# Performance work log

Measured on AMD Instinct MI355X. Metric: run time of the kernel, lower is better.

Reference implementation:

```python
import jax, jax.numpy as jnp
import numpy as np

EMBED = 1024
HEADS = 16
HEAD_DIM = EMBED // HEADS
N, SEQ = 8, 1024


def setup_inputs() -> dict:
    key = jax.random.key(0)
    ks = jax.random.split(key, 9)
    values = jax.random.normal(ks[0], (N, SEQ, EMBED), dtype=jnp.float32)
    keys_ = jax.random.normal(ks[1], (N, SEQ, EMBED), dtype=jnp.float32)
    query = jax.random.normal(ks[2], (N, SEQ, EMBED), dtype=jnp.float32)
    mask = jax.random.randint(ks[3], (N, 1, SEQ, SEQ), 0, 2, dtype=jnp.int32)
    s = 1.0 / np.sqrt(HEAD_DIM)
    Wv = jax.random.normal(ks[4], (HEAD_DIM, HEAD_DIM), dtype=jnp.float32) * s
    Wk = jax.random.normal(ks[5], (HEAD_DIM, HEAD_DIM), dtype=jnp.float32) * s
    Wq = jax.random.normal(ks[6], (HEAD_DIM, HEAD_DIM), dtype=jnp.float32) * s
    Wo = jax.random.normal(ks[7], (EMBED, EMBED), dtype=jnp.float32) * (1.0 / np.sqrt(EMBED))
    bo = jax.random.normal(ks[8], (EMBED,), dtype=jnp.float32) * 0.01
    return {"values": values, "keys": keys_, "query": query, "mask": mask,
            "Wv": Wv, "Wk": Wk, "Wq": Wq, "Wo": Wo, "bo": bo}


def reference(values, keys, query, mask, Wv, Wk, Wq, Wo, bo):
    n, q_len = query.shape[0], query.shape[1]
    v_len, k_len = values.shape[1], keys.shape[1]
    # reshape to (N, len, H, Dh); per-head linear projections share a (Dh,Dh) weight.
    v = values.reshape(n, v_len, HEADS, HEAD_DIM)
    k = keys.reshape(n, k_len, HEADS, HEAD_DIM)
    q = query.reshape(n, q_len, HEADS, HEAD_DIM)
    # torch Linear: x @ W.T
    v = jnp.einsum('nlhd,ed->nlhe', v, Wv)
    k = jnp.einsum('nlhd,ed->nlhe', k, Wk)
    q = jnp.einsum('nlhd,ed->nlhe', q, Wq)
    # scores (N,H,Q,K); mask BEFORE scaling, exactly as the torch module does
    att = jnp.einsum('nqhd,nkhd->nhqk', q, k)
    att = jnp.where(mask == 0, jnp.float32(-1e20), att)
    att = jax.nn.softmax(att / jnp.sqrt(jnp.float32(EMBED)), axis=3)
    out = jnp.einsum('nhql,nlhd->nqhd', att, v).reshape(n, q_len, EMBED)
    return out @ Wo.T + bo
```

## Files before the change

kernel.cpp:

```cpp
#include <hip/hip_runtime.h>
#include <hip/hip_bf16.h>

using bf16x8 = __attribute__((ext_vector_type(8))) __bf16;
using f32x4  = __attribute__((ext_vector_type(4))) float;

#define NB 8
#define SEQ 1024
#define HEADS 16
#define HD 64
#define EMB 1024

#if __has_builtin(__builtin_amdgcn_exp2f)
  #define EXPD(x) __builtin_amdgcn_exp2f(x)
  #define QSCALE  0.04508422f
  #define MASKV  -4.5084e18f
#else
  #define EXPD(x) __expf(x)
  #define QSCALE  0.03125f
  #define MASKV  -3.125e18f
#endif

__device__ __forceinline__ int cvtpk_bf16(float lo, float hi) {
    int r;
    asm("v_cvt_pk_bf16_f32 %0, %1, %2" : "=v"(r) : "v"(lo), "v"(hi));
    return r;
}

__device__ __forceinline__ void gld16(const __bf16* g, __bf16* l) {
    __builtin_amdgcn_global_load_lds((const __attribute__((address_space(1))) void*)g,
                                     (__attribute__((address_space(3))) void*)l, 16, 0, 0);
}

__global__ __launch_bounds__(256) void mask_pack(const int* __restrict__ mask,
                                                 unsigned long long* __restrict__ mp)
{
    const int row = blockIdx.x, n = blockIdx.y, t = threadIdx.x;
    const int w = t >> 6, lane = t & 63;
    const int* m = mask + ((size_t)n * SEQ + row) * SEQ;
    #pragma unroll
    for (int i = 0; i < 4; ++i) {
        unsigned long long b = __ballot(m[i * 256 + w * 64 + lane] != 0);
        if (lane == 0) mp[((size_t)n * SEQ + row) * 16 + i * 4 + w] = b;
    }
}

__global__ __launch_bounds__(256, 4) void proj_mfma(
    const float* __restrict__ q_in, const float* __restrict__ k_in, const float* __restrict__ v_in,
    const float* __restrict__ Wq, const float* __restrict__ Wk, const float* __restrict__ Wv,
    __bf16* __restrict__ qp, __bf16* __restrict__ kp, __bf16* __restrict__ vpt)
{
    const int z = blockIdx.z;
    const float* X  = (z == 0) ? q_in : (z == 1) ? k_in : v_in;
    const float* Wf = (z == 0) ? Wq   : (z == 1) ? Wk   : Wv;

    __shared__ __align__(16) __bf16 Wb[64 * 72];
    __shared__ __align__(16) __bf16 Xb[64 * 72];
    const int t = threadIdx.x;
    const int nh = blockIdx.y, n = nh >> 4, h = nh & 15;
    const int l0 = blockIdx.x * 64;
    for (int i = t; i < 4096; i += 256)
        Wb[(i >> 6) * 72 + (i & 63)] = (__bf16)Wf[i];
    {
        const int row = t >> 2, seg = (t & 3) * 16;
        const float* src = X + ((size_t)(n * SEQ + l0 + row)) * EMB + h * 64 + seg;
        union { __bf16 b[16]; uint4 u[2]; } tmp;
        #pragma unroll
        for (int jj = 0; jj < 4; ++jj) {
            float4 f = ((const float4*)src)[jj];
            tmp.b[jj*4+0] = (__bf16)f.x; tmp.b[jj*4+1] = (__bf16)f.y;
            tmp.b[jj*4+2] = (__bf16)f.z; tmp.b[jj*4+3] = (__bf16)f.w;
        }
        *(uint4*)&Xb[row * 72 + seg]     = tmp.u[0];
        *(uint4*)&Xb[row * 72 + seg + 8] = tmp.u[1];
    }
    __syncthreads();
    const int w = t >> 6, lane = t & 63, quad = lane >> 4, lr = lane & 15;
    bf16x8 af[2];
    #pragma unroll
    for (int ks = 0; ks < 2; ++ks)
        af[ks] = *(const bf16x8*)&Xb[(w * 16 + lr) * 72 + ks * 32 + quad * 8];
    const f32x4 zero4 = {0.f, 0.f, 0.f, 0.f};
    f32x4 acc[4];
    #pragma unroll
    for (int et = 0; et < 4; ++et) {
        acc[et] = zero4;
        #pragma unroll
        for (int ks = 0; ks < 2; ++ks) {
            bf16x8 bfrag = *(const bf16x8*)&Wb[(et * 16 + lr) * 72 + ks * 32 + quad * 8];
            acc[et] = __builtin_amdgcn_mfma_f32_16x16x32_bf16(af[ks], bfrag, acc[et], 0, 0, 0);
        }
    }
    if (z == 0) {
        #pragma unroll
        for (int et = 0; et < 4; ++et) acc[et] *= QSCALE;
    }
    __syncthreads();
    if (z < 2) {
        #pragma unroll
        for (int et = 0; et < 4; ++et)
            #pragma unroll
            for (int rr = 0; rr < 4; ++rr)
                Xb[(w * 16 + quad * 4 + rr) * 72 + et * 16 + lr] = (__bf16)acc[et][rr];
        __syncthreads();
        const int row = t >> 2, seg = (t & 3) * 16;
        uint4 a = *(uint4*)&Xb[row * 72 + seg];
        uint4 b = *(uint4*)&Xb[row * 72 + seg + 8];
        __bf16* outp = (z == 0) ? qp : kp;
        __bf16* dst = outp + (size_t)nh * 65536 + (size_t)(l0 + row) * 64 + seg;
        *(uint4*)&dst[0] = a;
        *(uint4*)&dst[8] = b;
    } else {
        #pragma unroll
        for (int et = 0; et < 4; ++et)
            #pragma unroll
            for (int rr = 0; rr < 4; ++rr)
                Xb[(et * 16 + lr) * 72 + w * 16 + quad * 4 + rr] = (__bf16)acc[et][rr];
        __syncthreads();
        const int e = t >> 2, seg = (t & 3) * 16;
        uint4 a = *(uint4*)&Xb[e * 72 + seg];
        uint4 b = *(uint4*)&Xb[e * 72 + seg + 8];
        __bf16* dst = vpt + (size_t)nh * 65536 + (size_t)e * SEQ + l0 + seg;
        *(uint4*)&dst[0] = a;
        *(uint4*)&dst[8] = b;
    }
}

__global__ __launch_bounds__(256, 4) void attn_mfma(
    const __bf16* __restrict__ qp, const __bf16* __restrict__ kp, const __bf16* __restrict__ vpt,
    const unsigned long long* __restrict__ mp, __bf16* __restrict__ attn_out)
{
    __shared__ __align__(16) __bf16 KV[2][2][64 * 64];
    const int t = threadIdx.x, w = t >> 6, lane = t & 63, quad = lane >> 4, lr = lane & 15;
    const int bid = blockIdx.x;
    const int nh = bid & 127, qg = bid >> 7;
    const int n = nh >> 4, h = nh & 15;
    const int q0 = qg * 128;
    const __bf16* Q  = qp  + (size_t)nh * 65536;
    const __bf16* K  = kp  + (size_t)nh * 65536;
    const __bf16* VT = vpt + (size_t)nh * 65536;

    int qrow[2];
    bf16x8 qf[2][2];
    const unsigned long long* mrow[2];
    #pragma unroll
    for (int g = 0; g < 2; ++g) {
        qrow[g] = q0 + g * 64 + w * 16 + lr;
        qf[g][0] = *(const bf16x8*)&Q[(size_t)qrow[g] * 64 + quad * 8];
        qf[g][1] = *(const bf16x8*)&Q[(size_t)qrow[g] * 64 + 32 + quad * 8];
        mrow[g] = mp + ((size_t)n * SEQ + qrow[g]) * 16;
    }

    const int srow = t >> 3, sc8 = t & 7;
    const int sswz = (sc8 ^ (srow & 7)) * 8;
    const int kofs = srow * 64 + sswz;
    const int vofs = srow * SEQ + sswz;

    auto issue = [&](int kc) {
        const int b = kc & 1;
        __bf16* kb = (__bf16*)&KV[b][0][0];
        __bf16* vb = (__bf16*)&KV[b][1][0];
        const __bf16* ksrc = K  + (size_t)kc * 4096 + kofs;
        const __bf16* vsrc = VT + (size_t)kc * 64   + vofs;
        gld16(ksrc,            kb + t * 8);
        gld16(ksrc + 32 * 64,  kb + t * 8 + 2048);
        gld16(vsrc,            vb + t * 8);
        gld16(vsrc + 32 * SEQ, vb + t * 8 + 2048);
    };

    const int s0 = ((quad ^ (lr & 7))) * 8;
    const int s1 = s0 ^ 32;

    const f32x4 zero4 = {0.f, 0.f, 0.f, 0.f};
    f32x4 O[2][4];
    #pragma unroll
    for (int g = 0; g < 2; ++g)
        #pragma unroll
        for (int mt = 0; mt < 4; ++mt) O[g][mt] = zero4;
    float l_part[2] = {0.f, 0.f};

    issue(0);
    for (int kc = 0; kc < 16; ++kc) {
        __syncthreads();
        if (kc + 1 < 16) issue(kc + 1);
        const unsigned long long mw0 = mrow[0][kc], mw1 = mrow[1][kc];
        const __bf16* Kb = (const __bf16*)&KV[kc & 1][0][0];
        const __bf16* Vb = (const __bf16*)&KV[kc & 1][1][0];

        f32x4 S[2][4];
        #pragma unroll
        for (int g = 0; g < 2; ++g)
            #pragma unroll
            for (int kt = 0; kt < 4; ++kt) S[g][kt] = zero4;
        __builtin_amdgcn_s_setprio(1);
        #pragma unroll
        for (int kt = 0; kt < 4; ++kt) {
            bf16x8 kf0 = *(const bf16x8*)&Kb[(kt * 16 + lr) * 64 + s0];
            bf16x8 kf1 = *(const bf16x8*)&Kb[(kt * 16 + lr) * 64 + s1];
            S[0][kt] = __builtin_amdgcn_mfma_f32_16x16x32_bf16(kf0, qf[0][0], S[0][kt], 0, 0, 0);
            S[1][kt] = __builtin_amdgcn_mfma_f32_16x16x32_bf16(kf0, qf[1][0], S[1][kt], 0, 0, 0);
            S[0][kt] = __builtin_amdgcn_mfma_f32_16x16x32_bf16(kf1, qf[0][1], S[0][kt], 0, 0, 0);
            S[1][kt] = __builtin_amdgcn_mfma_f32_16x16x32_bf16(kf1, qf[1][1], S[1][kt], 0, 0, 0);
        }
        __builtin_amdgcn_s_setprio(0);

        bf16x8 pf[2][2];
        #pragma unroll
        for (int g = 0; g < 2; ++g) {
            const unsigned long long mword = g ? mw1 : mw0;
            const unsigned int mlo = (unsigned int)(mword >> (quad * 4));
            const unsigned int mhi = (unsigned int)(mword >> (32 + quad * 4));
            float ev[16];
            float lsum = 0.f;
            #pragma unroll
            for (int kt = 0; kt < 4; ++kt)
                #pragma unroll
                for (int r = 0; r < 4; ++r) {
                    unsigned int bits = (kt < 2) ? mlo : mhi;
                    int sh = (kt & 1) * 16 + r;
                    float sv = ((bits >> sh) & 1u) ? S[g][kt][r] : MASKV;
                    float e = EXPD(sv);
                    lsum += e;
                    ev[kt * 4 + r] = e;
                }
            l_part[g] += lsum;
            #pragma unroll
            for (int ks = 0; ks < 2; ++ks) {
                const int ka = (2 * ks) * 4, kb2 = (2 * ks + 1) * 4;
                int d0 = cvtpk_bf16(ev[ka + 0], ev[ka + 1]);
                int d1 = cvtpk_bf16(ev[ka + 2], ev[ka + 3]);
                int d2 = cvtpk_bf16(ev[kb2 + 0], ev[kb2 + 1]);
                int d3 = cvtpk_bf16(ev[kb2 + 2], ev[kb2 + 3]);
                asm("v_permlane32_swap_b32 %0, %1" : "+v"(d0), "+v"(d2));
                asm("v_permlane16_swap_b32 %0, %1" : "+v"(d0), "+v"(d2));
                asm("v_permlane32_swap_b32 %0, %1" : "+v"(d1), "+v"(d3));
                asm("v_permlane16_swap_b32 %0, %1" : "+v"(d1), "+v"(d3));
                union { int di[4]; bf16x8 v; } pb;
                pb.di[0] = d0; pb.di[1] = d1; pb.di[2] = d2; pb.di[3] = d3;
                pf[g][ks] = pb.v;
            }
        }

        __builtin_amdgcn_s_setprio(1);
        #pragma unroll
        for (int ks = 0; ks < 2; ++ks) {
            const int sv = ks ? s1 : s0;
            #pragma unroll
            for (int mt = 0; mt < 4; ++mt) {
                bf16x8 vf = *(const bf16x8*)&Vb[(mt * 16 + lr) * 64 + sv];
                O[0][mt] = __builtin_amdgcn_mfma_f32_16x16x32_bf16(vf, pf[0][ks], O[0][mt], 0, 0, 0);
                O[1][mt] = __builtin_amdgcn_mfma_f32_16x16x32_bf16(vf, pf[1][ks], O[1][mt], 0, 0, 0);
            }
        }
        __builtin_amdgcn_s_setprio(0);
    }
    #pragma unroll
    for (int g = 0; g < 2; ++g) {
        float l = l_part[g];
        l += __shfl_xor(l, 16, 64);
        l += __shfl_xor(l, 32, 64);
        const float linv = 1.0f / l;
        #pragma unroll
        for (int mt = 0; mt < 4; ++mt) {
            union { __bf16 b[4]; uint2 u; } pk;
            #pragma unroll
            for (int r = 0; r < 4; ++r) pk.b[r] = (__bf16)(O[g][mt][r] * linv);
            *(uint2*)&attn_out[((size_t)n * SEQ + qrow[g]) * EMB + h * 64 + mt * 16 + quad * 4] = pk.u;
        }
    }
}

__global__ __launch_bounds__(256) void cvt_wo(const float* __restrict__ Wo, __bf16* __restrict__ Wob)
{
    int i = blockIdx.x * 256 + threadIdx.x;
    float4 f = *(const float4*)&Wo[(size_t)i * 4];
    union { __bf16 b[4]; uint2 u; } tmp;
    tmp.b[0] = (__bf16)f.x; tmp.b[1] = (__bf16)f.y; tmp.b[2] = (__bf16)f.z; tmp.b[3] = (__bf16)f.w;
    *(uint2*)&Wob[(size_t)i * 4] = tmp.u;
}

__global__ __launch_bounds__(256, 4) void out_gemm_mfma(
    const __bf16* __restrict__ A, const __bf16* __restrict__ B,
    const float* __restrict__ bo, float* __restrict__ out)
{
    __shared__ __align__(16) __bf16 As[64 * 40];
    __shared__ __align__(16) __bf16 Bs[128 * 40];
    const int t = threadIdx.x, w = t >> 6, lane = t & 63, quad = lane >> 4, lr = lane & 15;
    const int wr = (w >> 1) * 32, wc = (w & 1) * 64;
    const int r0 = blockIdx.y * 64, e0 = blockIdx.x * 128;
    const f32x4 zero4 = {0.f, 0.f, 0.f, 0.f};
    f32x4 acc[2][4];
    #pragma unroll
    for (int mt = 0; mt < 2; ++mt)
        #pragma unroll
        for (int nt = 0; nt < 4; ++nt) acc[mt][nt] = zero4;
    for (int k0 = 0; k0 < 1024; k0 += 32) {
        __syncthreads();
        {
            int row = t >> 2, c8 = t & 3;
            *(uint4*)&As[row * 40 + c8 * 8] =
                *(const uint4*)&A[(size_t)(r0 + row) * EMB + k0 + c8 * 8];
        }
        for (int c = t; c < 512; c += 256) {
            int row = c >> 2, c8 = c & 3;
            *(uint4*)&Bs[row * 40 + c8 * 8] =
                *(const uint4*)&B[(size_t)(e0 + row) * EMB + k0 + c8 * 8];
        }
        __syncthreads();
        bf16x8 af[2], bf[4];
        #pragma unroll
        for (int mt = 0; mt < 2; ++mt)
            af[mt] = *(const bf16x8*)&As[(wr + mt * 16 + lr) * 40 + quad * 8];
        #pragma unroll
        for (int nt = 0; nt < 4; ++nt)
            bf[nt] = *(const bf16x8*)&Bs[(wc + nt * 16 + lr) * 40 + quad * 8];
        #pragma unroll
        for (int mt = 0; mt < 2; ++mt)
            #pragma unroll
            for (int nt = 0; nt < 4; ++nt)
                acc[mt][nt] = __builtin_amdgcn_mfma_f32_16x16x32_bf16(af[mt], bf[nt], acc[mt][nt], 0, 0, 0);
    }
    float bv[4];
    #pragma unroll
    for (int nt = 0; nt < 4; ++nt) bv[nt] = bo[e0 + wc + nt * 16 + lr];
    #pragma unroll
    for (int mt = 0; mt < 2; ++mt)
        #pragma unroll
        for (int nt = 0; nt < 4; ++nt)
            #pragma unroll
            for (int rr = 0; rr < 4; ++rr)
                out[(size_t)(r0 + wr + mt * 16 + quad * 4 + rr) * EMB + e0 + wc + nt * 16 + lr] =
                    acc[mt][nt][rr] + bv[nt];
}

extern "C" void kernel_launch(void* const* d_in, const int* in_sizes, int n_in,
                              void* d_out, int out_size, void* d_ws, size_t ws_size,
                              hipStream_t stream) {
    const float* values = (const float*)d_in[0];
    const float* keys   = (const float*)d_in[1];
    const float* query  = (const float*)d_in[2];
    const int*   mask   = (const int*)d_in[3];
    const float* Wv     = (const float*)d_in[4];
    const float* Wk     = (const float*)d_in[5];
    const float* Wq     = (const float*)d_in[6];
    const float* Wo     = (const float*)d_in[7];
    const float* bo     = (const float*)d_in[8];
    float* out = (float*)d_out;

    const size_t per = (size_t)NB * HEADS * SEQ * HD;
    __bf16* qp   = (__bf16*)d_ws;
    __bf16* kp   = qp + per;
    __bf16* vpt  = kp + per;
    __bf16* attn = vpt + per;
    __bf16* Wob  = attn + (size_t)NB * SEQ * EMB;
    unsigned long long* maskp = (unsigned long long*)(Wob + (size_t)EMB * EMB);

    mask_pack<<<dim3(SEQ, NB), 256, 0, stream>>>(mask, maskp);
    proj_mfma<<<dim3(16, 128, 3), 256, 0, stream>>>(query, keys, values, Wq, Wk, Wv, qp, kp, vpt);
    cvt_wo<<<1024, 256, 0, stream>>>(Wo, Wob);
    attn_mfma<<<1024, 256, 0, stream>>>(qp, kp, vpt, maskp, attn);
    out_gemm_mfma<<<dim3(EMB / 128, NB * SEQ / 64), 256, 0, stream>>>(attn, Wob, bo, out);
}
```

Before: 278.3 us.

## Pre-permute mask into wave-uniform lane masks and select exp via cndmask

```diff
diff --git a/kernel.cpp b/kernel.cpp
--- a/kernel.cpp
+++ b/kernel.cpp
@@ -3,6 +3,7 @@
 
 using bf16x8 = __attribute__((ext_vector_type(8))) __bf16;
 using f32x4  = __attribute__((ext_vector_type(4))) float;
+using f32x2  = __attribute__((ext_vector_type(2))) float;
 
 #define NB 8
 #define SEQ 1024
@@ -13,11 +14,9 @@
 #if __has_builtin(__builtin_amdgcn_exp2f)
   #define EXPD(x) __builtin_amdgcn_exp2f(x)
   #define QSCALE  0.04508422f
-  #define MASKV  -4.5084e18f
 #else
   #define EXPD(x) __expf(x)
   #define QSCALE  0.03125f
-  #define MASKV  -3.125e18f
 #endif
 
 __device__ __forceinline__ int cvtpk_bf16(float lo, float hi) {
@@ -26,22 +25,34 @@
     return r;
 }
 
+__device__ __forceinline__ float sel0(float e, unsigned long long m) {
+    float r;
+    asm("v_cndmask_b32 %0, 0, %1, %2" : "=v"(r) : "v"(e), "s"(m));
+    return r;
+}
+
 __device__ __forceinline__ void gld16(const __bf16* g, __bf16* l) {
     __builtin_amdgcn_global_load_lds((const __attribute__((address_space(1))) void*)g,
                                      (__attribute__((address_space(3))) void*)l, 16, 0, 0);
 }
 
-__global__ __launch_bounds__(256) void mask_pack(const int* __restrict__ mask,
-                                                 unsigned long long* __restrict__ mp)
-{
-    const int row = blockIdx.x, n = blockIdx.y, t = threadIdx.x;
-    const int w = t >> 6, lane = t & 63;
-    const int* m = mask + ((size_t)n * SEQ + row) * SEQ;
-    #pragma unroll
-    for (int i = 0; i < 4; ++i) {
-        unsigned long long b = __ballot(m[i * 256 + w * 64 + lane] != 0);
-        if (lane == 0) mp[((size_t)n * SEQ + row) * 16 + i * 4 + w] = b;
-    }
+__global__ __launch_bounds__(256) void mask_perm(const int* __restrict__ mask,
+                                                 unsigned long long* __restrict__ mq)
+{
+    const int t = threadIdx.x, w = t >> 6, lane = t & 63, quad = lane >> 4, lq = lane & 15;
+    const int bx = blockIdx.x;
+    const int n = blockIdx.y;
+    const int qg = bx >> 5, g = (bx >> 4) & 1, kc = bx & 15;
+    const int q = qg * 128 + g * 64 + w * 16 + lq;
+    const int* mrow = mask + ((size_t)n * SEQ + q) * SEQ + kc * 64 + quad * 4;
+    unsigned long long* dst = mq + ((size_t)(((n * 8 + qg) * 4 + w) * 2 + g) * 16 + kc) * 16;
+    #pragma unroll
+    for (int kt = 0; kt < 4; ++kt)
+        #pragma unroll
+        for (int r = 0; r < 4; ++r) {
+            unsigned long long b = __ballot(mrow[kt * 16 + r] != 0);
+            if (lane == 0) dst[kt * 4 + r] = b;
+        }
 }
 
 __global__ __launch_bounds__(256, 4) void proj_mfma(
@@ -127,7 +138,7 @@
 
 __global__ __launch_bounds__(256, 4) void attn_mfma(
     const __bf16* __restrict__ qp, const __bf16* __restrict__ kp, const __bf16* __restrict__ vpt,
-    const unsigned long long* __restrict__ mp, __bf16* __restrict__ attn_out)
+    const unsigned long long* __restrict__ mq, __bf16* __restrict__ attn_out)
 {
     __shared__ __align__(16) __bf16 KV[2][2][64 * 64];
     const int t = threadIdx.x, w = t >> 6, lane = t & 63, quad = lane >> 4, lr = lane & 15;
@@ -139,15 +150,16 @@
     const __bf16* K  = kp  + (size_t)nh * 65536;
     const __bf16* VT = vpt + (size_t)nh * 65536;
 
+    const int wu = __builtin_amdgcn_readfirstlane(w);
+    const unsigned long long* mq_w = mq + (size_t)((n * 8 + qg) * 4 + wu) * 512;
+
     int qrow[2];
     bf16x8 qf[2][2];
-    const unsigned long long* mrow[2];
     #pragma unroll
     for (int g = 0; g < 2; ++g) {
         qrow[g] = q0 + g * 64 + w * 16 + lr;
         qf[g][0] = *(const bf16x8*)&Q[(size_t)qrow[g] * 64 + quad * 8];
         qf[g][1] = *(const bf16x8*)&Q[(size_t)qrow[g] * 64 + 32 + quad * 8];
-        mrow[g] = mp + ((size_t)n * SEQ + qrow[g]) * 16;
     }
 
     const int srow = t >> 3, sc8 = t & 7;
@@ -176,13 +188,12 @@
     for (int g = 0; g < 2; ++g)
         #pragma unroll
         for (int mt = 0; mt < 4; ++mt) O[g][mt] = zero4;
-    float l_part[2] = {0.f, 0.f};
+    f32x2 lp2[2] = {{0.f, 0.f}, {0.f, 0.f}};
 
     issue(0);
     for (int kc = 0; kc < 16; ++kc) {
         __syncthreads();
         if (kc + 1 < 16) issue(kc + 1);
-        const unsigned long long mw0 = mrow[0][kc], mw1 = mrow[1][kc];
         const __bf16* Kb = (const __bf16*)&KV[kc & 1][0][0];
         const __bf16* Vb = (const __bf16*)&KV[kc & 1][1][0];
 
@@ -206,23 +217,18 @@
         bf16x8 pf[2][2];
         #pragma unroll
         for (int g = 0; g < 2; ++g) {
-            const unsigned long long mword = g ? mw1 : mw0;
-            const unsigned int mlo = (unsigned int)(mword >> (quad * 4));
-            const unsigned int mhi = (unsigned int)(mword >> (32 + quad * 4));
+            const unsigned long long* Mg = mq_w + g * 256 + kc * 16;
             float ev[16];
-            float lsum = 0.f;
             #pragma unroll
             for (int kt = 0; kt < 4; ++kt)
                 #pragma unroll
-                for (int r = 0; r < 4; ++r) {
-                    unsigned int bits = (kt < 2) ? mlo : mhi;
-                    int sh = (kt & 1) * 16 + r;
-                    float sv = ((bits >> sh) & 1u) ? S[g][kt][r] : MASKV;
-                    float e = EXPD(sv);
-                    lsum += e;
-                    ev[kt * 4 + r] = e;
-                }
-            l_part[g] += lsum;
+                for (int r = 0; r < 4; ++r)
+                    ev[kt * 4 + r] = sel0(EXPD(S[g][kt][r]), Mg[kt * 4 + r]);
+            #pragma unroll
+            for (int i = 0; i < 8; ++i) {
+                f32x2 p2 = {ev[2 * i], ev[2 * i + 1]};
+                lp2[g] += p2;
+            }
             #pragma unroll
             for (int ks = 0; ks < 2; ++ks) {
                 const int ka = (2 * ks) * 4, kb2 = (2 * ks + 1) * 4;
@@ -255,7 +261,7 @@
     }
     #pragma unroll
     for (int g = 0; g < 2; ++g) {
-        float l = l_part[g];
+        float l = lp2[g].x + lp2[g].y;
         l += __shfl_xor(l, 16, 64);
         l += __shfl_xor(l, 32, 64);
         const float linv = 1.0f / l;
@@ -352,11 +358,11 @@
     __bf16* vpt  = kp + per;
     __bf16* attn = vpt + per;
     __bf16* Wob  = attn + (size_t)NB * SEQ * EMB;
-    unsigned long long* maskp = (unsigned long long*)(Wob + (size_t)EMB * EMB);
-
-    mask_pack<<<dim3(SEQ, NB), 256, 0, stream>>>(mask, maskp);
+    unsigned long long* maskq = (unsigned long long*)(Wob + (size_t)EMB * EMB);
+
+    mask_perm<<<dim3(256, NB), 256, 0, stream>>>(mask, maskq);
     proj_mfma<<<dim3(16, 128, 3), 256, 0, stream>>>(query, keys, values, Wq, Wk, Wv, qp, kp, vpt);
     cvt_wo<<<1024, 256, 0, stream>>>(Wo, Wob);
-    attn_mfma<<<1024, 256, 0, stream>>>(qp, kp, vpt, maskp, attn);
+    attn_mfma<<<1024, 256, 0, stream>>>(qp, kp, vpt, maskq, attn);
     out_gemm_mfma<<<dim3(EMB / 128, NB * SEQ / 64), 256, 0, stream>>>(attn, Wob, bo, out);
 }
```

After: 278.2 us. About the same (-0.1%).
